# Kernel optimization log

Hardware: AMD Instinct MI355X
Metric: run time of the kernel (lower is better)

## Reference

```python
import jax, jax.numpy as jnp
import numpy as np

B, S_ENC, S_DEC, ENC_H, DEC_H = 8, 2048, 2048, 512, 512


def setup_inputs() -> dict:
    key = jax.random.key(0)
    k1, k2, k3 = jax.random.split(key, 3)
    return {
        "enc_hidden_states": jax.random.normal(k1, (B, S_ENC, ENC_H), dtype=jnp.float32),
        "dec_hidden_states": jax.random.normal(k2, (B, S_DEC, DEC_H), dtype=jnp.float32),
        "W_att": jax.random.normal(k3, (ENC_H, DEC_H), dtype=jnp.float32),
    }


def reference(enc_hidden_states, dec_hidden_states, W_att):
    # Project encoder states: [B, S_enc, dec_h]
    enc_proj = jnp.einsum("bse,ed->bsd", enc_hidden_states, W_att)
    # Luong 'general' scores for all decoder timesteps at once: [B, S_dec, S_enc]
    # (original code loops over decoder timesteps via tf.map_fn; this is the
    # equivalent single batched matmul)
    att_logits = jnp.einsum("btd,bsd->bts", dec_hidden_states, enc_proj)
    att_softmax = jax.nn.softmax(att_logits, axis=-1)
    # Attention context vectors: [B, S_dec, enc_h]
    att_vector = jnp.einsum("bts,bse->bte", att_softmax, enc_hidden_states)
    return att_vector
```

## Files before the change

### kernel.cpp

```cpp
#include <hip/hip_runtime.h>
#include <cstdint>


#define DEVINL __device__ __forceinline__

typedef __attribute__((ext_vector_type(8))) short short8;
typedef __attribute__((ext_vector_type(4))) float f32x4;

DEVINL short f2bf(float x) {
    union { float f; uint32_t u; } v; v.f = x;
    uint32_t r = v.u + 0x7FFFu + ((v.u >> 16) & 1u);
    return (short)(r >> 16);
}
DEVINL float bf2f(short h) {
    union { uint32_t u; float f; } v; v.u = ((uint32_t)(uint16_t)h) << 16;
    return v.f;
}

DEVINL void gload_lds16(const void* g, void* l) {
    __builtin_amdgcn_global_load_lds(
        (const __attribute__((address_space(1))) char*)g,
        (__attribute__((address_space(3))) char*)l, 16, 0, 0);
}

__global__ __launch_bounds__(256)
void split_w_kernel(const float* __restrict__ w, short* __restrict__ wth,
                    short* __restrict__ wtl)
{
    int idx = blockIdx.x * 256 + threadIdx.x;
    int k = idx >> 9, n = idx & 511;
    float v = w[idx];
    short h = f2bf(v);
    wth[(long)n * 512 + k] = h;
    wtl[(long)n * 512 + k] = f2bf(v - bf2f(h));
}

__global__ __launch_bounds__(256)
void split_transpose_kernel(const float* __restrict__ x, short* __restrict__ hi,
                            short* __restrict__ lo, short* __restrict__ xt)
{
    __shared__ short tile[32][33];
    const int b  = blockIdx.z;
    const int s0 = blockIdx.x * 32;
    const int e0 = blockIdx.y * 32;
    const float* px = x + (long)b * 2048 * 512;
    short* ph = hi + (long)b * 2048 * 512;
    short* pl = lo + (long)b * 2048 * 512;
    short* pt = xt + (long)b * 512 * 2048;
    const int tx = threadIdx.x & 31;
    const int ty = threadIdx.x >> 5;
#pragma unroll
    for (int r = 0; r < 32; r += 8) {
        long idx = (long)(s0 + ty + r) * 512 + e0 + tx;
        float v = px[idx];
        short h = f2bf(v);
        ph[idx] = h;
        pl[idx] = f2bf(v - bf2f(h));
        tile[ty + r][tx] = h;
    }
    __syncthreads();
#pragma unroll
    for (int r = 0; r < 32; r += 8)
        pt[(long)(e0 + ty + r) * 2048 + s0 + tx] = tile[tx][ty + r];
}

template<int NTERMS, bool SPLIT_OUT>
__global__ __launch_bounds__(256, 2)
void gemm_bt(const short* __restrict__ Ah, const short* __restrict__ Al,
             const short* __restrict__ Bh, const short* __restrict__ Bl,
             float* __restrict__ C, short* __restrict__ Ch, short* __restrict__ Cl,
             int K, int lda, int ldb, int ldc,
             long sA, long sB, long sC)
{
    extern __shared__ char smem_raw[];
    constexpr int OPS = (NTERMS == 3) ? 4 : 2;
    constexpr int SET = 128 * 32 * OPS;
    short* smem = (short*)smem_raw;

    const int tid  = threadIdx.x;
    const int wave = tid >> 6;
    const int lane = tid & 63;
    const int quad = lane >> 4;
    const int l16  = lane & 15;
    const int wm   = (wave >> 1) * 64;
    const int wn   = (wave & 1) * 64;

    const long tile_m = (long)blockIdx.y * 128;
    const long tile_n = (long)blockIdx.x * 128;
    const int  bz     = blockIdx.z;

    const short* pAh = Ah + (long)bz * sA;
    const short* pBh = Bh + (long)bz * sB;
    const short* pAl = (NTERMS == 3) ? (Al + (long)bz * sA) : nullptr;
    const short* pBl = (NTERMS == 3) ? (Bl + (long)bz * sB) : nullptr;

    const int srow = tid >> 2;
    const int skq  = (tid & 3) * 8;
    const int lds_off = srow * 32 + skq;
    const long ga0 = (tile_m + srow) * (long)lda + skq;
    const long gb0 = (tile_n + srow) * (long)ldb + skq;

    auto stage = [&](int k0, int buf) {
        short* s   = smem + buf * SET;
        short* ash = s;
        short* bsh = s + 128 * 32;
        gload_lds16(pAh + ga0 + k0,             ash + lds_off);
        gload_lds16(pAh + ga0 + 64l * lda + k0, ash + lds_off + 64 * 32);
        gload_lds16(pBh + gb0 + k0,             bsh + lds_off);
        gload_lds16(pBh + gb0 + 64l * ldb + k0, bsh + lds_off + 64 * 32);
        if constexpr (NTERMS == 3) {
            short* asl = s + 2 * 128 * 32;
            short* bsl = s + 3 * 128 * 32;
            gload_lds16(pAl + ga0 + k0,             asl + lds_off);
            gload_lds16(pAl + ga0 + 64l * lda + k0, asl + lds_off + 64 * 32);
            gload_lds16(pBl + gb0 + k0,             bsl + lds_off);
            gload_lds16(pBl + gb0 + 64l * ldb + k0, bsl + lds_off + 64 * 32);
        }
    };

    f32x4 acc[4][4] = {};
    stage(0, 0);
    int cur = 0;

    for (int k0 = 0; k0 < K; k0 += 32) {
        __syncthreads();
        if (k0 + 32 < K) stage(k0 + 32, cur ^ 1);

        short* s   = smem + cur * SET;
        short* ash = s;
        short* bsh = s + 128 * 32;
        short* asl = s + 2 * 128 * 32;
        short* bsl = s + 3 * 128 * 32;

        short8 ah[4], bh[4], al[4], bl[4];
#pragma unroll
        for (int i = 0; i < 4; i++) {
            ah[i] = *(const short8*)&ash[(wm + i * 16 + l16) * 32 + quad * 8];
            bh[i] = *(const short8*)&bsh[(wn + i * 16 + l16) * 32 + quad * 8];
            if constexpr (NTERMS == 3) {
                al[i] = *(const short8*)&asl[(wm + i * 16 + l16) * 32 + quad * 8];
                bl[i] = *(const short8*)&bsl[(wn + i * 16 + l16) * 32 + quad * 8];
            }
        }
#pragma unroll
        for (int i = 0; i < 4; i++)
#pragma unroll
            for (int j = 0; j < 4; j++) {
                acc[i][j] = __builtin_amdgcn_mfma_f32_16x16x32_bf16(ah[i], bh[j], acc[i][j], 0, 0, 0);
                if constexpr (NTERMS == 3) {
                    acc[i][j] = __builtin_amdgcn_mfma_f32_16x16x32_bf16(ah[i], bl[j], acc[i][j], 0, 0, 0);
                    acc[i][j] = __builtin_amdgcn_mfma_f32_16x16x32_bf16(al[i], bh[j], acc[i][j], 0, 0, 0);
                }
            }
        cur ^= 1;
    }

#pragma unroll
    for (int i = 0; i < 4; i++)
#pragma unroll
        for (int j = 0; j < 4; j++) {
            const long row0 = tile_m + wm + i * 16 + quad * 4;
            const long col  = tile_n + wn + j * 16 + l16;
#pragma unroll
            for (int r = 0; r < 4; r++) {
                float v = acc[i][j][r];
                if constexpr (SPLIT_OUT) {
                    long idx = (long)bz * sC + (row0 + r) * (long)ldc + col;
                    short h = f2bf(v);
                    Ch[idx] = h;
                    Cl[idx] = f2bf(v - bf2f(h));
                } else {
                    C[(long)bz * sC + (row0 + r) * (long)ldc + col] = v;
                }
            }
        }
}

__global__ __launch_bounds__(512, 2)
void gemm3_256(const float* __restrict__ Dec, const short* __restrict__ Bh,
               const short* __restrict__ Bl, short* __restrict__ Pt,
               float* __restrict__ stats, int nbx, int nby)
{
    extern __shared__ char smem_raw[];
    short* smem = (short*)smem_raw;
    constexpr int PL  = 256 * 32;
    constexpr int SET = 4 * PL;

    const int t    = threadIdx.x;
    const int wave = t >> 6;
    const int lane = t & 63;
    const int quad = lane >> 4;
    const int l16  = lane & 15;
    const int wm   = (wave >> 2) * 128;
    const int wn   = (wave & 3) * 64;
    const int kslot8 = ((quad ^ ((l16 >> 1) & 3)) << 3);

    const int nwg = gridDim.x;
    const int wg  = blockIdx.x;
    const int swz = (wg & 7) * (nwg >> 3) + (wg >> 3);
    const int per_b = nbx * nby;
    const int bz  = swz / per_b;
    const int rem = swz - bz * per_b;
    const long tile_m = (long)(rem / nbx) * 256;
    const long tile_n = (long)(rem % nbx) * 256;

    const float* pDec = Dec + (long)bz * 2048 * 512;
    const short* pBh  = Bh + (long)bz * 2048 * 512;
    const short* pBl  = Bl + (long)bz * 2048 * 512;

    const int srow   = t >> 2;
    const int schunk = (t & 3) ^ ((t >> 3) & 3);
    const long gB  = (tile_n + srow) * 512l + schunk * 8;
    const long gB2 = gB + 128l * 512;
    const int ld0 = t * 8;

    const int srowA = t >> 1;
    const int kA0   = (t & 1) * 16;
    const long gAf  = (tile_m + srowA) * 512l + kA0;
    const int xrA   = (srowA >> 1) & 3;
    const int c0    = kA0 >> 3;
    const int wA0   = srowA * 32 + ((c0 ^ xrA) << 3);
    const int wA1   = srowA * 32 + (((c0 + 1) ^ xrA) << 3);

    f32x4 af[4];
    auto loadA = [&](int k0) {
#pragma unroll
        for (int q = 0; q < 4; q++)
            af[q] = *(const f32x4*)(pDec + gAf + k0 + q * 4);
    };
    auto writeA = [&](int buf) {
        short8 h0, h1, l0, l1;
#pragma unroll
        for (int e = 0; e < 8; e++) {
            float v = af[e >> 2][e & 3];
            short hh = f2bf(v);
            h0[e] = hh; l0[e] = f2bf(v - bf2f(hh));
        }
#pragma unroll
        for (int e = 0; e < 8; e++) {
            float v = af[2 + (e >> 2)][e & 3];
            short hh = f2bf(v);
            h1[e] = hh; l1[e] = f2bf(v - bf2f(hh));
        }
        short* sp = smem + buf * SET;
        *(short8*)&sp[wA0]      = h0;
        *(short8*)&sp[wA1]      = h1;
        *(short8*)&sp[PL + wA0] = l0;
        *(short8*)&sp[PL + wA1] = l1;
    };

    f32x4 acc[8][4] = {};

    loadA(0);
    __builtin_amdgcn_sched_barrier(0);
    gload_lds16(pBh + gB,  smem + 2 * PL + ld0);
    gload_lds16(pBh + gB2, smem + 2 * PL + ld0 + 4096);
    gload_lds16(pBl + gB,  smem + 3 * PL + ld0);
    gload_lds16(pBl + gB2, smem + 3 * PL + ld0 + 4096);
    __builtin_amdgcn_sched_barrier(0);
    asm volatile("s_waitcnt vmcnt(2)" ::: "memory");
    writeA(0);
    asm volatile("s_waitcnt lgkmcnt(0)" ::: "memory");
    __builtin_amdgcn_s_barrier();

    int cur = 0;
#pragma unroll 1
    for (int kt = 0; kt < 16; ++kt) {
        const short* s    = smem + cur * SET;
        short* sn         = smem + (cur ^ 1) * SET;
        const short* ah_p = s;
        const short* al_p = s + PL;
        const short* bh_p = s + 2 * PL;
        const short* bl_p = s + 3 * PL;
        const int  k0n  = (kt + 1) << 5;
        const bool more = (kt + 1 < 16);

        short8 ahA[4], ahB[4], xbh[4], xbl[4], xal[4];

#pragma unroll
        for (int i = 0; i < 4; i++)
            ahA[i] = *(const short8*)&ah_p[(wm + i * 16 + l16) * 32 + kslot8];
#pragma unroll
        for (int j = 0; j < 4; j++)
            xbh[j] = *(const short8*)&bh_p[(wn + j * 16 + l16) * 32 + kslot8];
        __builtin_amdgcn_s_barrier();
        asm volatile("s_waitcnt lgkmcnt(0)" ::: "memory");
        __builtin_amdgcn_sched_barrier(0);
        __builtin_amdgcn_s_setprio(1);
#pragma unroll
        for (int i = 0; i < 4; i++)
#pragma unroll
            for (int j = 0; j < 4; j++)
                acc[i][j] = __builtin_amdgcn_mfma_f32_16x16x32_bf16(ahA[i], xbh[j], acc[i][j], 0, 0, 0);
        __builtin_amdgcn_s_setprio(0);

#pragma unroll
        for (int i = 0; i < 4; i++)
            ahB[i] = *(const short8*)&ah_p[(wm + 64 + i * 16 + l16) * 32 + kslot8];
        if (more) {
            gload_lds16(pBh + gB  + k0n, sn + 2 * PL + ld0);
            gload_lds16(pBh + gB2 + k0n, sn + 2 * PL + ld0 + 4096);
        }
        __builtin_amdgcn_s_barrier();
        asm volatile("s_waitcnt lgkmcnt(0)" ::: "memory");
        __builtin_amdgcn_sched_barrier(0);
        __builtin_amdgcn_s_setprio(1);
#pragma unroll
        for (int i = 0; i < 4; i++)
#pragma unroll
            for (int j = 0; j < 4; j++)
                acc[4 + i][j] = __builtin_amdgcn_mfma_f32_16x16x32_bf16(ahB[i], xbh[j], acc[4 + i][j], 0, 0, 0);
        __builtin_amdgcn_s_setprio(0);

#pragma unroll
        for (int i = 0; i < 4; i++)
            xal[i] = *(const short8*)&al_p[(wm + i * 16 + l16) * 32 + kslot8];
        if (more) {
            loadA(k0n);
            __builtin_amdgcn_sched_barrier(0);
            gload_lds16(pBl + gB  + k0n, sn + 3 * PL + ld0);
            gload_lds16(pBl + gB2 + k0n, sn + 3 * PL + ld0 + 4096);
        }
        __builtin_amdgcn_s_barrier();
        asm volatile("s_waitcnt lgkmcnt(0)" ::: "memory");
        __builtin_amdgcn_sched_barrier(0);
        __builtin_amdgcn_s_setprio(1);
#pragma unroll
        for (int i = 0; i < 4; i++)
#pragma unroll
            for (int j = 0; j < 4; j++)
                acc[i][j] = __builtin_amdgcn_mfma_f32_16x16x32_bf16(xal[i], xbh[j], acc[i][j], 0, 0, 0);
        __builtin_amdgcn_s_setprio(0);

#pragma unroll
        for (int i = 0; i < 4; i++)
            xal[i] = *(const short8*)&al_p[(wm + 64 + i * 16 + l16) * 32 + kslot8];
        if (more)
            asm volatile("s_waitcnt vmcnt(8)" ::: "memory");
        else
            asm volatile("s_waitcnt vmcnt(0)" ::: "memory");
        __builtin_amdgcn_s_barrier();
        asm volatile("s_waitcnt lgkmcnt(0)" ::: "memory");
        __builtin_amdgcn_sched_barrier(0);
        __builtin_amdgcn_s_setprio(1);
#pragma unroll
        for (int i = 0; i < 4; i++)
#pragma unroll
            for (int j = 0; j < 4; j++)
                acc[4 + i][j] = __builtin_amdgcn_mfma_f32_16x16x32_bf16(xal[i], xbh[j], acc[4 + i][j], 0, 0, 0);
        __builtin_amdgcn_s_setprio(0);

#pragma unroll
        for (int j = 0; j < 4; j++)
            xbl[j] = *(const short8*)&bl_p[(wn + j * 16 + l16) * 32 + kslot8];
        if (more) {
            asm volatile("s_waitcnt vmcnt(2)" ::: "memory");
            writeA(cur ^ 1);
        }
        __builtin_amdgcn_s_barrier();
        asm volatile("s_waitcnt lgkmcnt(0)" ::: "memory");
        __builtin_amdgcn_sched_barrier(0);
        __builtin_amdgcn_s_setprio(1);
#pragma unroll
        for (int i = 0; i < 4; i++)
#pragma unroll
            for (int j = 0; j < 4; j++)
                acc[i][j] = __builtin_amdgcn_mfma_f32_16x16x32_bf16(ahA[i], xbl[j], acc[i][j], 0, 0, 0);
        __builtin_amdgcn_s_setprio(0);

        __builtin_amdgcn_s_setprio(1);
#pragma unroll
        for (int i = 0; i < 4; i++)
#pragma unroll
            for (int j = 0; j < 4; j++)
                acc[4 + i][j] = __builtin_amdgcn_mfma_f32_16x16x32_bf16(ahB[i], xbl[j], acc[4 + i][j], 0, 0, 0);
        __builtin_amdgcn_s_setprio(0);
        if (more)
            __builtin_amdgcn_s_barrier();

        cur ^= 1;
    }

    float* sf   = (float*)smem_raw;
    float* lmax = sf;
    float* rowm = sf + 1024;
    const int wr = wave >> 2, wc = wave & 3;
    __syncthreads();

#pragma unroll
    for (int i = 0; i < 8; i++)
#pragma unroll
        for (int r = 0; r < 4; r++) {
            float m = acc[i][0][r];
#pragma unroll
            for (int j = 1; j < 4; j++) m = fmaxf(m, acc[i][j][r]);
#pragma unroll
            for (int o = 1; o < 16; o <<= 1) m = fmaxf(m, __shfl_xor(m, o));
            if (l16 == 0) lmax[wc * 256 + wr * 128 + i * 16 + quad * 4 + r] = m;
        }
    __syncthreads();
    if (t < 256)
        rowm[t] = fmaxf(fmaxf(lmax[t], lmax[256 + t]),
                        fmaxf(lmax[512 + t], lmax[768 + t]));
    __syncthreads();
    float* lsum = sf;
    short* PtB  = Pt + (long)bz * 2048 * 2048;
#pragma unroll
    for (int i = 0; i < 8; i++)
#pragma unroll
        for (int r = 0; r < 4; r++) {
            const int rit = wr * 128 + i * 16 + quad * 4 + r;
            const float m = rowm[rit];
            float sum = 0.f;
#pragma unroll
            for (int j = 0; j < 4; j++) {
                float e = __expf(acc[i][j][r] - m);
                sum += e;
                PtB[(tile_m + rit) * 2048 + tile_n + wn + j * 16 + l16] = f2bf(e);
            }
#pragma unroll
            for (int o = 1; o < 16; o <<= 1) sum += __shfl_xor(sum, o);
            if (l16 == 0) lsum[wc * 256 + rit] = sum;
        }
    __syncthreads();
    if (t < 256) {
        float S = lsum[t] + lsum[256 + t] + lsum[512 + t] + lsum[768 + t];
        const long sidx = (((long)bz * 2048 + tile_m + t) * 8 + (tile_n >> 8)) * 2;
        stats[sidx]     = rowm[t];
        stats[sidx + 1] = S;
    }
}

__global__ __launch_bounds__(256)
void combine_kernel(const float* __restrict__ stats, float* __restrict__ scales)
{
    const long row = (long)blockIdx.x * 256 + threadIdx.x;
    const float* p = stats + row * 16;
    float m[8], s[8];
#pragma unroll
    for (int t = 0; t < 8; t++) { m[t] = p[t * 2]; s[t] = p[t * 2 + 1]; }
    float M = m[0];
#pragma unroll
    for (int t = 1; t < 8; t++) M = fmaxf(M, m[t]);
    float S = 0.f;
#pragma unroll
    for (int t = 0; t < 8; t++) S += s[t] * __expf(m[t] - M);
    const float inv = 1.f / S;
#pragma unroll
    for (int t = 0; t < 8; t++)
        scales[row * 8 + t] = __expf(m[t] - M) * inv;
}

__global__ __launch_bounds__(256, 2)
void gemm_pv(const short* __restrict__ A, const short* __restrict__ B,
             const float* __restrict__ scales, float* __restrict__ C,
             int K, int lda, int ldb, int ldc,
             long sA, long sB, long sC)
{
    extern __shared__ char smem_raw[];
    constexpr int SET = 128 * 32 * 2;
    short* smem = (short*)smem_raw;

    const int tid  = threadIdx.x;
    const int wave = tid >> 6;
    const int lane = tid & 63;
    const int quad = lane >> 4;
    const int l16  = lane & 15;
    const int wm   = (wave >> 1) * 64;
    const int wn   = (wave & 1) * 64;

    const long tile_m = (long)blockIdx.y * 128;
    const long tile_n = (long)blockIdx.x * 128;
    const int  bz     = blockIdx.z;

    const short* pA = A + (long)bz * sA;
    const short* pB = B + (long)bz * sB;

    const int srow = tid >> 2;
    const int skq  = (tid & 3) * 8;
    const int lds_off = srow * 32 + skq;
    const long ga0 = (tile_m + srow) * (long)lda + skq;
    const long gb0 = (tile_n + srow) * (long)ldb + skq;

    auto stage = [&](int k0, int buf) {
        short* s   = smem + buf * SET;
        short* ash = s;
        short* bsh = s + 128 * 32;
        gload_lds16(pA + ga0 + k0,             ash + lds_off);
        gload_lds16(pA + ga0 + 64l * lda + k0, ash + lds_off + 64 * 32);
        gload_lds16(pB + gb0 + k0,             bsh + lds_off);
        gload_lds16(pB + gb0 + 64l * ldb + k0, bsh + lds_off + 64 * 32);
    };

    f32x4 acc[4][4] = {};
    f32x4 oacc[4][4] = {};
    const f32x4 vzero = {0.f, 0.f, 0.f, 0.f};
    stage(0, 0);
    int cur = 0;

    for (int k0 = 0; k0 < K; k0 += 32) {
        __syncthreads();
        if (k0 + 32 < K) stage(k0 + 32, cur ^ 1);

        short* s   = smem + cur * SET;
        short* ash = s;
        short* bsh = s + 128 * 32;

        short8 ah[4], bh[4];
#pragma unroll
        for (int i = 0; i < 4; i++) {
            ah[i] = *(const short8*)&ash[(wm + i * 16 + l16) * 32 + quad * 8];
            bh[i] = *(const short8*)&bsh[(wn + i * 16 + l16) * 32 + quad * 8];
        }
#pragma unroll
        for (int i = 0; i < 4; i++)
#pragma unroll
            for (int j = 0; j < 4; j++)
                acc[i][j] = __builtin_amdgcn_mfma_f32_16x16x32_bf16(ah[i], bh[j], acc[i][j], 0, 0, 0);

        if (((k0 + 32) & 255) == 0) {
            const int tt = k0 >> 8;
#pragma unroll
            for (int i = 0; i < 4; i++) {
                f32x4 sv;
#pragma unroll
                for (int r = 0; r < 4; r++)
                    sv[r] = scales[((long)bz * 2048 + tile_m + wm + i * 16 + quad * 4 + r) * 8 + tt];
#pragma unroll
                for (int j = 0; j < 4; j++) {
                    oacc[i][j] += sv * acc[i][j];
                    acc[i][j] = vzero;
                }
            }
        }
        cur ^= 1;
    }

#pragma unroll
    for (int i = 0; i < 4; i++)
#pragma unroll
        for (int j = 0; j < 4; j++) {
            const long row0 = tile_m + wm + i * 16 + quad * 4;
            const long col  = tile_n + wn + j * 16 + l16;
#pragma unroll
            for (int r = 0; r < 4; r++)
                C[(long)bz * sC + (row0 + r) * (long)ldc + col] = oacc[i][j][r];
        }
}

extern "C" void kernel_launch(void* const* d_in, const int* in_sizes, int n_in,
                              void* d_out, int out_size, void* d_ws, size_t ws_size,
                              hipStream_t stream)
{
    const float* enc = (const float*)d_in[0];
    const float* dec = (const float*)d_in[1];
    const float* W   = (const float*)d_in[2];
    float* out = (float*)d_out;

    const long BSE = 8l * 2048 * 512;
    const long NW  = 512l * 512;

    char* p = (char*)d_ws;
    auto take = [&](long bytes) { char* r = p; p += (bytes + 255) & ~255l; return r; };
    short* enc_hi = (short*)take(BSE * 2);
    short* enc_lo = (short*)take(BSE * 2);
    short* ep_hi  = (short*)take(BSE * 2);
    short* ep_lo  = (short*)take(BSE * 2);
    short* enc_t  = (short*)take(BSE * 2);
    short* wt_hi  = (short*)take(NW * 2);
    short* wt_lo  = (short*)take(NW * 2);
    short* Pt     = (short*)take(8l * 2048 * 2048 * 2);
    float* stats  = (float*)take(8l * 2048 * 8 * 2 * 4);
    float* scales = (float*)take(8l * 2048 * 8 * 4);
    (void)ws_size; (void)in_sizes; (void)n_in; (void)out_size;

    static bool attr_set = false;
    if (!attr_set) {
        (void)hipFuncSetAttribute((const void*)gemm3_256,
                                  hipFuncAttributeMaxDynamicSharedMemorySize,
                                  131072);
        attr_set = true;
    }

    split_transpose_kernel<<<dim3(64, 16, 8), 256, 0, stream>>>(
        enc, enc_hi, enc_lo, enc_t);
    split_w_kernel<<<1024, 256, 0, stream>>>(W, wt_hi, wt_lo);

    gemm_bt<3, true><<<dim3(4, 128, 1), 256, 64 * 1024, stream>>>(
        enc_hi, enc_lo, wt_hi, wt_lo, nullptr, ep_hi, ep_lo,
        512, 512, 512, 512, 0, 0, 0);

    gemm3_256<<<512, 512, 131072, stream>>>(
        dec, ep_hi, ep_lo, Pt, stats, 8, 8);

    combine_kernel<<<64, 256, 0, stream>>>(stats, scales);

    gemm_pv<<<dim3(4, 16, 8), 256, 32 * 1024, stream>>>(
        Pt, enc_t, scales, out,
        2048, 2048, 2048, 512, 2048l * 2048, 512l * 2048, 2048l * 512);
}
```

Baseline: 372.0 us.

## Stage fp32 decoder tile via direct LDS loads and split to bf16 at fragment read

The A operand (fp32 decoder states) is now copied straight into LDS with global_load_lds instead of going through registers. Each wave then converts it to bf16 hi/lo pairs as it reads its MFMA fragments, which removes the register round-trip and the separate writeA conversion and store pass. Most intra-iteration barriers and lgkmcnt waits are dropped, and launch bounds change from 2 to 1 blocks per CU to allow more registers. The cost is duplicated conversion work across the waves that share rows, a larger LDS footprint from storing fp32, and lower occupancy.

```diff
diff --git a/kernel.cpp b/kernel.cpp
--- a/kernel.cpp
+++ b/kernel.cpp
@@ -176,15 +176,15 @@
         }
 }
 
-__global__ __launch_bounds__(512, 2)
+__global__ __launch_bounds__(512, 1)
 void gemm3_256(const float* __restrict__ Dec, const short* __restrict__ Bh,
                const short* __restrict__ Bl, short* __restrict__ Pt,
                float* __restrict__ stats, int nbx, int nby)
 {
     extern __shared__ char smem_raw[];
     short* smem = (short*)smem_raw;
-    constexpr int PL  = 256 * 32;
-    constexpr int SET = 4 * PL;
+    constexpr int APL = 16384;
+    constexpr int SET = APL + 2 * 8192;
 
     const int t    = threadIdx.x;
     const int wave = t >> 6;
@@ -194,6 +194,9 @@
     const int wm   = (wave >> 2) * 128;
     const int wn   = (wave & 3) * 64;
     const int kslot8 = ((quad ^ ((l16 >> 1) & 3)) << 3);
+    const int x7   = l16 & 7;
+    const int c0f  = ((2 * quad) ^ x7) << 2;
+    const int c1f  = ((2 * quad + 1) ^ x7) << 2;
 
     const int nwg = gridDim.x;
     const int wg  = blockIdx.x;
@@ -214,53 +217,42 @@
     const long gB2 = gB + 128l * 512;
     const int ld0 = t * 8;
 
-    const int srowA = t >> 1;
-    const int kA0   = (t & 1) * 16;
-    const long gAf  = (tile_m + srowA) * 512l + kA0;
-    const int xrA   = (srowA >> 1) & 3;
-    const int c0    = kA0 >> 3;
-    const int wA0   = srowA * 32 + ((c0 ^ xrA) << 3);
-    const int wA1   = srowA * 32 + (((c0 + 1) ^ xrA) << 3);
-
-    f32x4 af[4];
-    auto loadA = [&](int k0) {
-#pragma unroll
-        for (int q = 0; q < 4; q++)
-            af[q] = *(const f32x4*)(pDec + gAf + k0 + q * 4);
+    const int arow = t >> 3;
+    const int agc  = (t & 7) ^ (arow & 7);
+    const long gAf = (tile_m + arow) * 512l + agc * 4;
+    const int ldA  = t * 8;
+
+    auto stageA = [&](int k0f, short* sp) {
+#pragma unroll
+        for (int p = 0; p < 4; p++)
+            gload_lds16(pDec + gAf + (long)p * 64 * 512 + k0f,
+                        sp + ldA + p * 4096);
     };
-    auto writeA = [&](int buf) {
-        short8 h0, h1, l0, l1;
-#pragma unroll
-        for (int e = 0; e < 8; e++) {
-            float v = af[e >> 2][e & 3];
-            short hh = f2bf(v);
-            h0[e] = hh; l0[e] = f2bf(v - bf2f(hh));
-        }
-#pragma unroll
-        for (int e = 0; e < 8; e++) {
-            float v = af[2 + (e >> 2)][e & 3];
-            short hh = f2bf(v);
-            h1[e] = hh; l1[e] = f2bf(v - bf2f(hh));
-        }
-        short* sp = smem + buf * SET;
-        *(short8*)&sp[wA0]      = h0;
-        *(short8*)&sp[wA1]      = h1;
-        *(short8*)&sp[PL + wA0] = l0;
-        *(short8*)&sp[PL + wA1] = l1;
+
+    auto rdA = [&](const float* fA, int row, short8& hi, short8& lo) {
+        f32x4 va = *(const f32x4*)&fA[row * 32 + c0f];
+        f32x4 vb = *(const f32x4*)&fA[row * 32 + c1f];
+#pragma unroll
+        for (int e = 0; e < 4; e++) {
+            short h = f2bf(va[e]); hi[e] = h; lo[e] = f2bf(va[e] - bf2f(h));
+        }
+#pragma unroll
+        for (int e = 0; e < 4; e++) {
+            short h = f2bf(vb[e]); hi[4 + e] = h; lo[4 + e] = f2bf(vb[e] - bf2f(h));
+        }
     };
 
     f32x4 acc[8][4] = {};
 
-    loadA(0);
+    stageA(0, smem);
     __builtin_amdgcn_sched_barrier(0);
-    gload_lds16(pBh + gB,  smem + 2 * PL + ld0);
-    gload_lds16(pBh + gB2, smem + 2 * PL + ld0 + 4096);
-    gload_lds16(pBl + gB,  smem + 3 * PL + ld0);
-    gload_lds16(pBl + gB2, smem + 3 * PL + ld0 + 4096);
+    gload_lds16(pBh + gB,  smem + APL + ld0);
+    gload_lds16(pBh + gB2, smem + APL + ld0 + 4096);
+    __builtin_amdgcn_sched_barrier(0);
+    gload_lds16(pBl + gB,  smem + APL + 8192 + ld0);
+    gload_lds16(pBl + gB2, smem + APL + 8192 + ld0 + 4096);
     __builtin_amdgcn_sched_barrier(0);
     asm volatile("s_waitcnt vmcnt(2)" ::: "memory");
-    writeA(0);
-    asm volatile("s_waitcnt lgkmcnt(0)" ::: "memory");
     __builtin_amdgcn_s_barrier();
 
     int cur = 0;
@@ -268,115 +260,96 @@
     for (int kt = 0; kt < 16; ++kt) {
         const short* s    = smem + cur * SET;
         short* sn         = smem + (cur ^ 1) * SET;
-        const short* ah_p = s;
-        const short* al_p = s + PL;
-        const short* bh_p = s + 2 * PL;
-        const short* bl_p = s + 3 * PL;
+        const float* fA   = (const float*)s;
+        const short* bh_p = s + APL;
+        const short* bl_p = s + APL + 8192;
         const int  k0n  = (kt + 1) << 5;
         const bool more = (kt + 1 < 16);
 
-        short8 ahA[4], ahB[4], xbh[4], xbl[4], xal[4];
-
-#pragma unroll
-        for (int i = 0; i < 4; i++)
-            ahA[i] = *(const short8*)&ah_p[(wm + i * 16 + l16) * 32 + kslot8];
+        short8 hi0[4], lo0[4], hi1[4], lo1[4], xbh[4], xbl[4];
+
+#pragma unroll
+        for (int i = 0; i < 4; i++)
+            rdA(fA, wm + i * 16 + l16, hi0[i], lo0[i]);
 #pragma unroll
         for (int j = 0; j < 4; j++)
             xbh[j] = *(const short8*)&bh_p[(wn + j * 16 + l16) * 32 + kslot8];
-        __builtin_amdgcn_s_barrier();
-        asm volatile("s_waitcnt lgkmcnt(0)" ::: "memory");
-        __builtin_amdgcn_sched_barrier(0);
+        if (more) {
+            stageA(k0n, sn);
+            __builtin_amdgcn_sched_barrier(0);
+        }
         __builtin_amdgcn_s_setprio(1);
 #pragma unroll
         for (int i = 0; i < 4; i++)
 #pragma unroll
             for (int j = 0; j < 4; j++)
-                acc[i][j] = __builtin_amdgcn_mfma_f32_16x16x32_bf16(ahA[i], xbh[j], acc[i][j], 0, 0, 0);
+                acc[i][j] = __builtin_amdgcn_mfma_f32_16x16x32_bf16(hi0[i], xbh[j], acc[i][j], 0, 0, 0);
         __builtin_amdgcn_s_setprio(0);
 
 #pragma unroll
         for (int i = 0; i < 4; i++)
-            ahB[i] = *(const short8*)&ah_p[(wm + 64 + i * 16 + l16) * 32 + kslot8];
+            rdA(fA, wm + 64 + i * 16 + l16, hi1[i], lo1[i]);
         if (more) {
-            gload_lds16(pBh + gB  + k0n, sn + 2 * PL + ld0);
-            gload_lds16(pBh + gB2 + k0n, sn + 2 * PL + ld0 + 4096);
-        }
-        __builtin_amdgcn_s_barrier();
-        asm volatile("s_waitcnt lgkmcnt(0)" ::: "memory");
-        __builtin_amdgcn_sched_barrier(0);
+            gload_lds16(pBh + gB  + k0n, sn + APL + ld0);
+            gload_lds16(pBh + gB2 + k0n, sn + APL + ld0 + 4096);
+            __builtin_amdgcn_sched_barrier(0);
+        }
         __builtin_amdgcn_s_setprio(1);
 #pragma unroll
         for (int i = 0; i < 4; i++)
 #pragma unroll
             for (int j = 0; j < 4; j++)
-                acc[4 + i][j] = __builtin_amdgcn_mfma_f32_16x16x32_bf16(ahB[i], xbh[j], acc[4 + i][j], 0, 0, 0);
+                acc[4 + i][j] = __builtin_amdgcn_mfma_f32_16x16x32_bf16(hi1[i], xbh[j], acc[4 + i][j], 0, 0, 0);
         __builtin_amdgcn_s_setprio(0);
 
-#pragma unroll
-        for (int i = 0; i < 4; i++)
-            xal[i] = *(const short8*)&al_p[(wm + i * 16 + l16) * 32 + kslot8];
         if (more) {
-            loadA(k0n);
+            gload_lds16(pBl + gB  + k0n, sn + APL + 8192 + ld0);
+            gload_lds16(pBl + gB2 + k0n, sn + APL + 8192 + ld0 + 4096);
             __builtin_amdgcn_sched_barrier(0);
-            gload_lds16(pBl + gB  + k0n, sn + 3 * PL + ld0);
-            gload_lds16(pBl + gB2 + k0n, sn + 3 * PL + ld0 + 4096);
-        }
-        __builtin_amdgcn_s_barrier();
-        asm volatile("s_waitcnt lgkmcnt(0)" ::: "memory");
-        __builtin_amdgcn_sched_barrier(0);
+        }
         __builtin_amdgcn_s_setprio(1);
 #pragma unroll
         for (int i = 0; i < 4; i++)
 #pragma unroll
             for (int j = 0; j < 4; j++)
-                acc[i][j] = __builtin_amdgcn_mfma_f32_16x16x32_bf16(xal[i], xbh[j], acc[i][j], 0, 0, 0);
+                acc[i][j] = __builtin_amdgcn_mfma_f32_16x16x32_bf16(lo0[i], xbh[j], acc[i][j], 0, 0, 0);
         __builtin_amdgcn_s_setprio(0);
 
-#pragma unroll
-        for (int i = 0; i < 4; i++)
-            xal[i] = *(const short8*)&al_p[(wm + 64 + i * 16 + l16) * 32 + kslot8];
+        __builtin_amdgcn_s_setprio(1);
+#pragma unroll
+        for (int i = 0; i < 4; i++)
+#pragma unroll
+            for (int j = 0; j < 4; j++)
+                acc[4 + i][j] = __builtin_amdgcn_mfma_f32_16x16x32_bf16(lo1[i], xbh[j], acc[4 + i][j], 0, 0, 0);
+        __builtin_amdgcn_s_setprio(0);
         if (more)
             asm volatile("s_waitcnt vmcnt(8)" ::: "memory");
         else
             asm volatile("s_waitcnt vmcnt(0)" ::: "memory");
         __builtin_amdgcn_s_barrier();
-        asm volatile("s_waitcnt lgkmcnt(0)" ::: "memory");
-        __builtin_amdgcn_sched_barrier(0);
-        __builtin_amdgcn_s_setprio(1);
-#pragma unroll
-        for (int i = 0; i < 4; i++)
-#pragma unroll
-            for (int j = 0; j < 4; j++)
-                acc[4 + i][j] = __builtin_amdgcn_mfma_f32_16x16x32_bf16(xal[i], xbh[j], acc[4 + i][j], 0, 0, 0);
-        __builtin_amdgcn_s_setprio(0);
 
 #pragma unroll
         for (int j = 0; j < 4; j++)
             xbl[j] = *(const short8*)&bl_p[(wn + j * 16 + l16) * 32 + kslot8];
+        __builtin_amdgcn_s_setprio(1);
+#pragma unroll
+        for (int i = 0; i < 4; i++)
+#pragma unroll
+            for (int j = 0; j < 4; j++)
+                acc[i][j] = __builtin_amdgcn_mfma_f32_16x16x32_bf16(hi0[i], xbl[j], acc[i][j], 0, 0, 0);
+        __builtin_amdgcn_s_setprio(0);
+
+        __builtin_amdgcn_s_setprio(1);
+#pragma unroll
+        for (int i = 0; i < 4; i++)
+#pragma unroll
+            for (int j = 0; j < 4; j++)
+                acc[4 + i][j] = __builtin_amdgcn_mfma_f32_16x16x32_bf16(hi1[i], xbl[j], acc[4 + i][j], 0, 0, 0);
+        __builtin_amdgcn_s_setprio(0);
         if (more) {
             asm volatile("s_waitcnt vmcnt(2)" ::: "memory");
-            writeA(cur ^ 1);
-        }
-        __builtin_amdgcn_s_barrier();
-        asm volatile("s_waitcnt lgkmcnt(0)" ::: "memory");
-        __builtin_amdgcn_sched_barrier(0);
-        __builtin_amdgcn_s_setprio(1);
-#pragma unroll
-        for (int i = 0; i < 4; i++)
-#pragma unroll
-            for (int j = 0; j < 4; j++)
-                acc[i][j] = __builtin_amdgcn_mfma_f32_16x16x32_bf16(ahA[i], xbl[j], acc[i][j], 0, 0, 0);
-        __builtin_amdgcn_s_setprio(0);
-
-        __builtin_amdgcn_s_setprio(1);
-#pragma unroll
-        for (int i = 0; i < 4; i++)
-#pragma unroll
-            for (int j = 0; j < 4; j++)
-                acc[4 + i][j] = __builtin_amdgcn_mfma_f32_16x16x32_bf16(ahB[i], xbl[j], acc[4 + i][j], 0, 0, 0);
-        __builtin_amdgcn_s_setprio(0);
-        if (more)
             __builtin_amdgcn_s_barrier();
+        }
 
         cur ^= 1;
     }
```

After: 700.2 us. 88.2% more time.
